# Performance work log

Hardware: AMD Instinct MI355X
Metric: run time of the kernel (lower is better)

## Reference

```python
import jax, jax.numpy as jnp
import numpy as np

C = 256
CQK = C // 8  # query/key channel dim from Conv3d(in, in//8, 1)


def setup_inputs() -> dict:
    key = jax.random.key(0)
    ks = jax.random.split(key, 8)
    B, D, H, W = 2, 16, 16, 16
    x = jax.random.normal(ks[0], (B, C, D, H, W), dtype=jnp.float32)
    s = 1.0 / np.sqrt(C)
    q_w = jax.random.normal(ks[1], (CQK, C), dtype=jnp.float32) * s
    q_b = jax.random.normal(ks[2], (CQK,), dtype=jnp.float32) * 0.01
    k_w = jax.random.normal(ks[3], (CQK, C), dtype=jnp.float32) * s
    k_b = jax.random.normal(ks[4], (CQK,), dtype=jnp.float32) * 0.01
    v_w = jax.random.normal(ks[5], (C, C), dtype=jnp.float32) * s
    v_b = jax.random.normal(ks[6], (C,), dtype=jnp.float32) * 0.01
    gamma = jax.random.normal(ks[7], (1,), dtype=jnp.float32)
    return {"x": x, "q_w": q_w, "q_b": q_b, "k_w": k_w, "k_b": k_b,
            "v_w": v_w, "v_b": v_b, "gamma": gamma}


def reference(x, q_w, q_b, k_w, k_b, v_w, v_b, gamma):
    B, Cc, D, H, W = x.shape
    N = D * H * W
    xf = x.reshape(B, Cc, N)  # [B, C, N]
    # 1x1x1 Conv3d == channel-mixing matmul
    q = jnp.einsum('oc,bcn->bon', q_w, xf) + q_b[None, :, None]  # [B, C/8, N]
    k = jnp.einsum('oc,bcn->bon', k_w, xf) + k_b[None, :, None]  # [B, C/8, N]
    v = jnp.einsum('oc,bcn->bon', v_w, xf) + v_b[None, :, None]  # [B, C, N]
    # attention[b, i, j] = sum_c q[b, c, i] * k[b, c, j]
    attn = jnp.einsum('bci,bcj->bij', q, k)  # [B, N, N]
    attn = jax.nn.softmax(attn, axis=-1)
    # out[b, c, i] = sum_j v[b, c, j] * attn[b, i, j]
    out = jnp.einsum('bcj,bij->bci', v, attn)  # [B, C, N]
    out = out.reshape(B, Cc, D, H, W)
    return gamma[0] * out + x
```

## Files before the change

kernel.cpp:

```cpp
#include <hip/hip_runtime.h>

#define C_DIM 256
#define CQK   32
#define N_DIM 4096
#define B_DIM 2

typedef __attribute__((ext_vector_type(8))) short bf16x8;
typedef __attribute__((ext_vector_type(4))) float f32x4;

__device__ __forceinline__ unsigned short f2bf(float f) {
    union { float f; unsigned u; } v; v.f = f;
    unsigned r = v.u + 0x7FFFu + ((v.u >> 16) & 1u);
    return (unsigned short)(r >> 16);
}
__device__ __forceinline__ unsigned pk2(float a, float b) {
    return (unsigned)f2bf(a) | ((unsigned)f2bf(b) << 16);
}
__device__ __forceinline__ unsigned pk2t(float a, float b) {
    union { float f; unsigned u; } ua, ub; ua.f = a; ub.f = b;
    return __builtin_amdgcn_perm(ub.u, ua.u, 0x07060302u);
}
#define EXP2(x) __builtin_amdgcn_exp2f(x)
#define MFMA(A, B, C) __builtin_amdgcn_mfma_f32_16x16x32_bf16((A), (B), (C), 0, 0, 0)

__global__ __launch_bounds__(256) void wconv(
    const float* __restrict__ q_w, const float* __restrict__ q_b,
    const float* __restrict__ k_w, const float* __restrict__ k_b,
    const float* __restrict__ v_w, const float* __restrict__ v_b,
    unsigned short* __restrict__ wbf, float* __restrict__ biasf)
{
    const float LOG2E = 1.4426950408889634f;
    int o = blockIdx.x, c = threadIdx.x;
    float w;
    if (o < 32)       w = q_w[o * C_DIM + c] * LOG2E;
    else if (o < 64)  w = k_w[(o - 32) * C_DIM + c];
    else              w = v_w[(o - 64) * C_DIM + c];
    wbf[o * C_DIM + c] = f2bf(w);
    if (c == 0) biasf[o] = (o < 32) ? q_b[o] * LOG2E
                         : (o < 64) ? k_b[o - 32] : v_b[o - 64];
}

__global__ __launch_bounds__(256, 2) void qkv_proj(
    const float* __restrict__ x, const unsigned short* __restrict__ wbf,
    const float* __restrict__ biasf,
    unsigned short* __restrict__ qT, unsigned short* __restrict__ kT,
    unsigned short* __restrict__ vbf)
{
    __shared__ __align__(16) unsigned short xsT[16 * 264];
    __shared__ __align__(16) unsigned short qkbuf[2][16 * 36];
    __shared__ __align__(16) unsigned short vbb[256 * 20];
    const int t  = threadIdx.x;
    const int b  = blockIdx.x >> 8;
    const int n0 = (blockIdx.x & 255) * 16;

    {
        int n4 = t & 3, cq = t >> 2;
        const float* xp = x + ((size_t)(b * C_DIM + cq * 4)) * N_DIM + n0 + n4 * 4;
        float4 r0 = *(const float4*)xp;
        float4 r1 = *(const float4*)(xp + N_DIM);
        float4 r2 = *(const float4*)(xp + 2 * N_DIM);
        float4 r3 = *(const float4*)(xp + 3 * N_DIM);
        float a0[4], a1[4], a2[4], a3[4];
        *(float4*)a0 = r0; *(float4*)a1 = r1; *(float4*)a2 = r2; *(float4*)a3 = r3;
        #pragma unroll
        for (int k = 0; k < 4; ++k) {
            uint2 pw;
            pw.x = pk2(a0[k], a1[k]);
            pw.y = pk2(a2[k], a3[k]);
            *(uint2*)&xsT[(n4 * 4 + k) * 264 + cq * 4] = pw;
        }
    }
    __syncthreads();

    const int w = t >> 6, lid = t & 63, lr = lid & 15, lq = lid >> 4;
    f32x4 acc[5] = {};
    #pragma unroll
    for (int ks = 0; ks < 8; ++ks) {
        bf16x8 xb = *(const bf16x8*)&xsT[lr * 264 + ks * 32 + lq * 8];
        #pragma unroll
        for (int u = 0; u < 5; ++u) {
            int gm = w * 5 + u;
            bf16x8 af = *(const bf16x8*)&wbf[(gm * 16 + lr) * C_DIM + ks * 32 + lq * 8];
            acc[u] = MFMA(af, xb, acc[u]);
        }
    }
    #pragma unroll
    for (int u = 0; u < 5; ++u) {
        int gm = w * 5 + u;
        float bv[4];
        *(float4*)bv = *(const float4*)&biasf[gm * 16 + lq * 4];
        if (gm >= 4) {
            int vc = (gm - 4) * 16 + lq * 4;
            #pragma unroll
            for (int r = 0; r < 4; ++r)
                vbb[(vc + r) * 20 + lr] = f2bf(acc[u][r] + bv[r]);
        } else {
            int sel = gm >> 1, half = gm & 1;
            uint2 pw;
            pw.x = pk2(acc[u][0] + bv[0], acc[u][1] + bv[1]);
            pw.y = pk2(acc[u][2] + bv[2], acc[u][3] + bv[3]);
            *(uint2*)&qkbuf[sel][lr * 36 + half * 16 + lq * 4] = pw;
        }
    }
    __syncthreads();
    if (t < 128) {
        int sel = t >> 6, idx = t & 63;
        int n = idx >> 2, ch8 = (idx & 3) * 8;
        const unsigned short* src = &qkbuf[sel][n * 36 + ch8];
        uint2 a = *(const uint2*)src;
        uint2 c = *(const uint2*)(src + 4);
        unsigned short* dst = (sel ? kT : qT) + ((size_t)b * N_DIM + n0 + n) * CQK + ch8;
        uint4 st; st.x = a.x; st.y = a.y; st.z = c.x; st.w = c.y;
        *(uint4*)dst = st;
    }
    {
        const unsigned short* src = &vbb[t * 20];
        uint2 a = *(const uint2*)(src + 0);
        uint2 bq = *(const uint2*)(src + 4);
        uint2 c = *(const uint2*)(src + 8);
        uint2 d = *(const uint2*)(src + 12);
        unsigned short* dst = vbf +
            ((((size_t)(b * 4 + (t >> 6)) * 128 + (n0 >> 5)) * 64 + (t & 63)) * 32
             + (n0 & 31));
        uint4 s0; s0.x = a.x; s0.y = a.y; s0.z = bq.x; s0.w = bq.y;
        uint4 s1; s1.x = c.x; s1.y = c.y; s1.z = d.x; s1.w = d.y;
        *(uint4*)dst = s0;
        *(uint4*)(dst + 8) = s1;
    }
}

__global__ __launch_bounds__(256, 2) void attn_kernel(
    const unsigned short* __restrict__ qT, const unsigned short* __restrict__ kT,
    const unsigned short* __restrict__ vbf, const float* __restrict__ x,
    const float* __restrict__ gamma, float* __restrict__ out)
{
    __shared__ __align__(16) char smem[40960 + 1536];
    unsigned short* pbase = (unsigned short*)smem;
    float* obuf = (float*)smem;
    float* lbuf = (float*)(smem + 40960);

    const int t  = threadIdx.x;
    const int b  = blockIdx.x >> 8;
    const int qt = (blockIdx.x >> 2) & 63;
    const int cs = blockIdx.x & 3;
    const int i0 = qt * 64;
    const int w = t >> 6, lid = t & 63, lr = lid & 15, lq = lid >> 4;

    const unsigned short* qTb = qT + (size_t)b * N_DIM * CQK;
    const unsigned short* kTb = kT + (size_t)b * N_DIM * CQK;
    const unsigned short* vtb = vbf + (size_t)(b * 4 + cs) * 128 * 2048;

    unsigned short* pW0 = pbase + (w * 2 + 0) * (64 * 40);
    unsigned short* pW1 = pbase + (w * 2 + 1) * (64 * 40);

    bf16x8 bq[4];
    #pragma unroll
    for (int it = 0; it < 4; ++it)
        bq[it] = *(const bf16x8*)&qTb[(i0 + it * 16 + lr) * CQK + lq * 8];

    f32x4 oa[4][4] = {};
    float lp[4] = {};

    const int jwbase = w * 1024;
    const int vlane = lr * 32 + lq * 8;

    bf16x8 akc0 = *(const bf16x8*)&kTb[(jwbase + lr) * CQK + lq * 8];
    bf16x8 akc1 = *(const bf16x8*)&kTb[(jwbase + 16 + lr) * CQK + lq * 8];
    bf16x8 avU[4];

    {
        const unsigned short* vt0 = vtb + (size_t)(w * 32) * 2048;
        #pragma unroll
        for (int ct = 0; ct < 4; ++ct)
            avU[ct] = *(const bf16x8*)&vt0[ct * 512 + vlane];
        bf16x8 akn0 = *(const bf16x8*)&kTb[(jwbase + 32 + lr) * CQK + lq * 8];
        bf16x8 akn1 = *(const bf16x8*)&kTb[(jwbase + 32 + 16 + lr) * CQK + lq * 8];
        const f32x4 z = {};
        #pragma unroll
        for (int it = 0; it < 4; ++it) {
            f32x4 s0 = MFMA(akc0, bq[it], z);
            f32x4 s1 = MFMA(akc1, bq[it], z);
            float e0 = EXP2(s0[0]), e1 = EXP2(s0[1]), e2 = EXP2(s0[2]), e3 = EXP2(s0[3]);
            float f0 = EXP2(s1[0]), f1 = EXP2(s1[1]), f2 = EXP2(s1[2]), f3 = EXP2(s1[3]);
            lp[it] += ((e0 + e1) + (e2 + e3)) + ((f0 + f1) + (f2 + f3));
            uint2 pw0; pw0.x = pk2t(e0, e1); pw0.y = pk2t(e2, e3);
            uint2 pw1; pw1.x = pk2t(f0, f1); pw1.y = pk2t(f2, f3);
            unsigned short* prow = pW0 + (it * 16 + lr) * 40;
            *(uint2*)&prow[lq * 4]      = pw0;
            *(uint2*)&prow[16 + lq * 4] = pw1;
        }
        akc0 = akn0; akc1 = akn1;
    }

    #pragma unroll 2
    for (int k = 1; k < 32; ++k) {
        const int jn = jwbase + ((k + 1) & 31) * 32;
        const unsigned short* vtk = vtb + (size_t)(w * 32 + k) * 2048;
        bf16x8 avI[4];
        #pragma unroll
        for (int ct = 0; ct < 4; ++ct)
            avI[ct] = *(const bf16x8*)&vtk[ct * 512 + vlane];
        bf16x8 akn0 = *(const bf16x8*)&kTb[(jn + lr) * CQK + lq * 8];
        bf16x8 akn1 = *(const bf16x8*)&kTb[(jn + 16 + lr) * CQK + lq * 8];
        const unsigned short* pR = (k & 1) ? pW0 : pW1;
        bf16x8 bp[4];
        #pragma unroll
        for (int it = 0; it < 4; ++it)
            bp[it] = *(const bf16x8*)&pR[(it * 16 + lr) * 40 + lq * 8];
        const f32x4 z = {};
        f32x4 s[4][2];
        #pragma unroll
        for (int it = 0; it < 4; ++it) {
            s[it][0] = MFMA(akc0, bq[it], z);
            s[it][1] = MFMA(akc1, bq[it], z);
        }
        #pragma unroll
        for (int it = 0; it < 4; ++it)
            #pragma unroll
            for (int ct = 0; ct < 4; ++ct)
                oa[ct][it] = MFMA(avU[ct], bp[it], oa[ct][it]);
        unsigned short* pWc = (k & 1) ? pW1 : pW0;
        #pragma unroll
        for (int it = 0; it < 4; ++it) {
            float e0 = EXP2(s[it][0][0]), e1 = EXP2(s[it][0][1]);
            float e2 = EXP2(s[it][0][2]), e3 = EXP2(s[it][0][3]);
            float f0 = EXP2(s[it][1][0]), f1 = EXP2(s[it][1][1]);
            float f2 = EXP2(s[it][1][2]), f3 = EXP2(s[it][1][3]);
            lp[it] += ((e0 + e1) + (e2 + e3)) + ((f0 + f1) + (f2 + f3));
            uint2 pw0; pw0.x = pk2t(e0, e1); pw0.y = pk2t(e2, e3);
            uint2 pw1; pw1.x = pk2t(f0, f1); pw1.y = pk2t(f2, f3);
            unsigned short* prow = pWc + (it * 16 + lr) * 40;
            *(uint2*)&prow[lq * 4]      = pw0;
            *(uint2*)&prow[16 + lq * 4] = pw1;
        }
        akc0 = akn0; akc1 = akn1;
        #pragma unroll
        for (int ct = 0; ct < 4; ++ct) avU[ct] = avI[ct];
    }

    {
        bf16x8 bp[4];
        #pragma unroll
        for (int it = 0; it < 4; ++it)
            bp[it] = *(const bf16x8*)&pW1[(it * 16 + lr) * 40 + lq * 8];
        #pragma unroll
        for (int it = 0; it < 4; ++it)
            #pragma unroll
            for (int ct = 0; ct < 4; ++ct)
                oa[ct][it] = MFMA(avU[ct], bp[it], oa[ct][it]);
    }

    #pragma unroll
    for (int it = 0; it < 4; ++it) {
        lp[it] += __shfl_xor(lp[it], 16);
        lp[it] += __shfl_xor(lp[it], 32);
    }
    if (lq == 0) {
        #pragma unroll
        for (int it = 0; it < 4; ++it)
            lbuf[w * 64 + it * 16 + lr] = lp[it];
    }
    __syncthreads();

    for (int ph = 0; ph < 4; ++ph) {
        if (w == ph) {
            #pragma unroll
            for (int ct = 0; ct < 4; ++ct)
                #pragma unroll
                for (int it = 0; it < 4; ++it)
                    #pragma unroll
                    for (int r = 0; r < 4; ++r) {
                        int addr = (ct * 16 + lq * 4 + r) * 68 + it * 16 + lr;
                        if (ph == 0) obuf[addr]  = oa[ct][it][r];
                        else         obuf[addr] += oa[ct][it][r];
                    }
        }
        __syncthreads();
    }
    if (t < 64) {
        float l = lbuf[t] + lbuf[64 + t] + lbuf[128 + t] + lbuf[192 + t];
        lbuf[256 + t] = 1.f / l;
    }
    __syncthreads();

    const float g = gamma[0];
    const int c0 = cs * 64;
    const int cc = t >> 2;
    const int ic = (t & 3) * 16;
    const size_t rowbase = ((size_t)b * C_DIM + c0 + cc) * N_DIM + i0 + ic;
    #pragma unroll
    for (int k = 0; k < 4; ++k) {
        float4 ov4 = *(const float4*)&obuf[cc * 68 + ic + k * 4];
        float4 li  = *(const float4*)&lbuf[256 + ic + k * 4];
        float4 xv  = *(const float4*)(x + rowbase + k * 4);
        float4 ov;
        ov.x = g * ov4.x * li.x + xv.x;
        ov.y = g * ov4.y * li.y + xv.y;
        ov.z = g * ov4.z * li.z + xv.z;
        ov.w = g * ov4.w * li.w + xv.w;
        *(float4*)(out + rowbase + k * 4) = ov;
    }
}

extern "C" void kernel_launch(void* const* d_in, const int* in_sizes, int n_in,
                              void* d_out, int out_size, void* d_ws, size_t ws_size,
                              hipStream_t stream) {
    const float* x     = (const float*)d_in[0];
    const float* q_w   = (const float*)d_in[1];
    const float* q_b   = (const float*)d_in[2];
    const float* k_w   = (const float*)d_in[3];
    const float* k_b   = (const float*)d_in[4];
    const float* v_w   = (const float*)d_in[5];
    const float* v_b   = (const float*)d_in[6];
    const float* gamma = (const float*)d_in[7];
    float* out = (float*)d_out;

    char* ws = (char*)d_ws;
    unsigned short* qT    = (unsigned short*)(ws);
    unsigned short* kT    = (unsigned short*)(ws + 524288);
    unsigned short* vbf   = (unsigned short*)(ws + 1048576);
    unsigned short* wbf   = (unsigned short*)(ws + 5242880);
    float*          biasf = (float*)(ws + 5406720);

    hipLaunchKernelGGL(wconv, dim3(320), dim3(256), 0, stream,
                       q_w, q_b, k_w, k_b, v_w, v_b, wbf, biasf);
    hipLaunchKernelGGL(qkv_proj, dim3(B_DIM * 256), dim3(256), 0, stream,
                       x, wbf, biasf, qT, kT, vbf);
    hipLaunchKernelGGL(attn_kernel, dim3(B_DIM * 64 * 4), dim3(256), 0, stream,
                       qT, kT, vbf, x, gamma, out);
}
```

Measured before the change: 122.5 us.

## Double query tile and wave count per attention block, drop software pipelining

The attention kernel now processes 128 queries per block with 8 waves (512 threads), each wave covering 512 keys instead of 1024. This halves the number of blocks and the redundant K/V loads per query. The double-buffered P tile and the software-pipelined loop, where the QK MFMA for step k overlapped the PV MFMA for step k-1, are replaced by a simple sequential loop with a single P buffer per wave. Costs are more accumulator registers (8 row tiles), lower occupancy from 512-thread blocks with a larger LDS footprint, less instruction-level overlap, and more serialized phases in the cross-wave output reduction.

```diff
diff --git a/kernel.cpp b/kernel.cpp
--- a/kernel.cpp
+++ b/kernel.cpp
@@ -129,55 +129,55 @@
     }
 }
 
-__global__ __launch_bounds__(256, 2) void attn_kernel(
+__global__ __launch_bounds__(512, 2) void attn_kernel(
     const unsigned short* __restrict__ qT, const unsigned short* __restrict__ kT,
     const unsigned short* __restrict__ vbf, const float* __restrict__ x,
     const float* __restrict__ gamma, float* __restrict__ out)
 {
-    __shared__ __align__(16) char smem[40960 + 1536];
+    __shared__ __align__(16) char smem[81920 + 4608];
     unsigned short* pbase = (unsigned short*)smem;
     float* obuf = (float*)smem;
-    float* lbuf = (float*)(smem + 40960);
+    float* lbuf = (float*)(smem + 81920);
 
     const int t  = threadIdx.x;
-    const int b  = blockIdx.x >> 8;
-    const int qt = (blockIdx.x >> 2) & 63;
+    const int b  = blockIdx.x >> 7;
+    const int qt = (blockIdx.x >> 2) & 31;
     const int cs = blockIdx.x & 3;
-    const int i0 = qt * 64;
+    const int i0 = qt * 128;
     const int w = t >> 6, lid = t & 63, lr = lid & 15, lq = lid >> 4;
 
     const unsigned short* qTb = qT + (size_t)b * N_DIM * CQK;
     const unsigned short* kTb = kT + (size_t)b * N_DIM * CQK;
     const unsigned short* vtb = vbf + (size_t)(b * 4 + cs) * 128 * 2048;
 
-    unsigned short* pW0 = pbase + (w * 2 + 0) * (64 * 40);
-    unsigned short* pW1 = pbase + (w * 2 + 1) * (64 * 40);
-
-    bf16x8 bq[4];
-    #pragma unroll
-    for (int it = 0; it < 4; ++it)
+    unsigned short* pW = pbase + w * (128 * 40);
+
+    bf16x8 bq[8];
+    #pragma unroll
+    for (int it = 0; it < 8; ++it)
         bq[it] = *(const bf16x8*)&qTb[(i0 + it * 16 + lr) * CQK + lq * 8];
 
-    f32x4 oa[4][4] = {};
-    float lp[4] = {};
-
-    const int jwbase = w * 1024;
+    f32x4 oa[4][8] = {};
+    float lp[8] = {};
+
+    const int jwbase = w * 512;
     const int vlane = lr * 32 + lq * 8;
 
     bf16x8 akc0 = *(const bf16x8*)&kTb[(jwbase + lr) * CQK + lq * 8];
     bf16x8 akc1 = *(const bf16x8*)&kTb[(jwbase + 16 + lr) * CQK + lq * 8];
-    bf16x8 avU[4];
-
-    {
-        const unsigned short* vt0 = vtb + (size_t)(w * 32) * 2048;
+
+    for (int k = 0; k < 16; ++k) {
+        const unsigned short* vtk = vtb + (size_t)(w * 16 + k) * 2048;
+        bf16x8 avU[4];
         #pragma unroll
         for (int ct = 0; ct < 4; ++ct)
-            avU[ct] = *(const bf16x8*)&vt0[ct * 512 + vlane];
-        bf16x8 akn0 = *(const bf16x8*)&kTb[(jwbase + 32 + lr) * CQK + lq * 8];
-        bf16x8 akn1 = *(const bf16x8*)&kTb[(jwbase + 32 + 16 + lr) * CQK + lq * 8];
+            avU[ct] = *(const bf16x8*)&vtk[ct * 512 + vlane];
+        const int jn = jwbase + ((k + 1) & 15) * 32;
+        bf16x8 akn0 = *(const bf16x8*)&kTb[(jn + lr) * CQK + lq * 8];
+        bf16x8 akn1 = *(const bf16x8*)&kTb[(jn + 16 + lr) * CQK + lq * 8];
         const f32x4 z = {};
         #pragma unroll
-        for (int it = 0; it < 4; ++it) {
+        for (int it = 0; it < 8; ++it) {
             f32x4 s0 = MFMA(akc0, bq[it], z);
             f32x4 s1 = MFMA(akc1, bq[it], z);
             float e0 = EXP2(s0[0]), e1 = EXP2(s0[1]), e2 = EXP2(s0[2]), e3 = EXP2(s0[3]);
@@ -185,113 +185,64 @@
             lp[it] += ((e0 + e1) + (e2 + e3)) + ((f0 + f1) + (f2 + f3));
             uint2 pw0; pw0.x = pk2t(e0, e1); pw0.y = pk2t(e2, e3);
             uint2 pw1; pw1.x = pk2t(f0, f1); pw1.y = pk2t(f2, f3);
-            unsigned short* prow = pW0 + (it * 16 + lr) * 40;
+            unsigned short* prow = pW + (it * 16 + lr) * 40;
             *(uint2*)&prow[lq * 4]      = pw0;
             *(uint2*)&prow[16 + lq * 4] = pw1;
         }
-        akc0 = akn0; akc1 = akn1;
-    }
-
-    #pragma unroll 2
-    for (int k = 1; k < 32; ++k) {
-        const int jn = jwbase + ((k + 1) & 31) * 32;
-        const unsigned short* vtk = vtb + (size_t)(w * 32 + k) * 2048;
-        bf16x8 avI[4];
-        #pragma unroll
-        for (int ct = 0; ct < 4; ++ct)
-            avI[ct] = *(const bf16x8*)&vtk[ct * 512 + vlane];
-        bf16x8 akn0 = *(const bf16x8*)&kTb[(jn + lr) * CQK + lq * 8];
-        bf16x8 akn1 = *(const bf16x8*)&kTb[(jn + 16 + lr) * CQK + lq * 8];
-        const unsigned short* pR = (k & 1) ? pW0 : pW1;
-        bf16x8 bp[4];
-        #pragma unroll
-        for (int it = 0; it < 4; ++it)
-            bp[it] = *(const bf16x8*)&pR[(it * 16 + lr) * 40 + lq * 8];
-        const f32x4 z = {};
-        f32x4 s[4][2];
-        #pragma unroll
-        for (int it = 0; it < 4; ++it) {
-            s[it][0] = MFMA(akc0, bq[it], z);
-            s[it][1] = MFMA(akc1, bq[it], z);
-        }
-        #pragma unroll
-        for (int it = 0; it < 4; ++it)
+        #pragma unroll
+        for (int it = 0; it < 8; ++it) {
+            bf16x8 bp = *(const bf16x8*)&pW[(it * 16 + lr) * 40 + lq * 8];
             #pragma unroll
             for (int ct = 0; ct < 4; ++ct)
-                oa[ct][it] = MFMA(avU[ct], bp[it], oa[ct][it]);
-        unsigned short* pWc = (k & 1) ? pW1 : pW0;
-        #pragma unroll
-        for (int it = 0; it < 4; ++it) {
-            float e0 = EXP2(s[it][0][0]), e1 = EXP2(s[it][0][1]);
-            float e2 = EXP2(s[it][0][2]), e3 = EXP2(s[it][0][3]);
-            float f0 = EXP2(s[it][1][0]), f1 = EXP2(s[it][1][1]);
-            float f2 = EXP2(s[it][1][2]), f3 = EXP2(s[it][1][3]);
-            lp[it] += ((e0 + e1) + (e2 + e3)) + ((f0 + f1) + (f2 + f3));
-            uint2 pw0; pw0.x = pk2t(e0, e1); pw0.y = pk2t(e2, e3);
-            uint2 pw1; pw1.x = pk2t(f0, f1); pw1.y = pk2t(f2, f3);
-            unsigned short* prow = pWc + (it * 16 + lr) * 40;
-            *(uint2*)&prow[lq * 4]      = pw0;
-            *(uint2*)&prow[16 + lq * 4] = pw1;
+                oa[ct][it] = MFMA(avU[ct], bp, oa[ct][it]);
         }
         akc0 = akn0; akc1 = akn1;
-        #pragma unroll
-        for (int ct = 0; ct < 4; ++ct) avU[ct] = avI[ct];
-    }
-
-    {
-        bf16x8 bp[4];
-        #pragma unroll
-        for (int it = 0; it < 4; ++it)
-            bp[it] = *(const bf16x8*)&pW1[(it * 16 + lr) * 40 + lq * 8];
-        #pragma unroll
-        for (int it = 0; it < 4; ++it)
-            #pragma unroll
-            for (int ct = 0; ct < 4; ++ct)
-                oa[ct][it] = MFMA(avU[ct], bp[it], oa[ct][it]);
-    }
-
-    #pragma unroll
-    for (int it = 0; it < 4; ++it) {
+    }
+
+    #pragma unroll
+    for (int it = 0; it < 8; ++it) {
         lp[it] += __shfl_xor(lp[it], 16);
         lp[it] += __shfl_xor(lp[it], 32);
     }
     if (lq == 0) {
         #pragma unroll
-        for (int it = 0; it < 4; ++it)
-            lbuf[w * 64 + it * 16 + lr] = lp[it];
-    }
-    __syncthreads();
-
-    for (int ph = 0; ph < 4; ++ph) {
+        for (int it = 0; it < 8; ++it)
+            lbuf[w * 128 + it * 16 + lr] = lp[it];
+    }
+    __syncthreads();
+
+    for (int ph = 0; ph < 8; ++ph) {
         if (w == ph) {
             #pragma unroll
             for (int ct = 0; ct < 4; ++ct)
                 #pragma unroll
-                for (int it = 0; it < 4; ++it)
+                for (int it = 0; it < 8; ++it)
                     #pragma unroll
                     for (int r = 0; r < 4; ++r) {
-                        int addr = (ct * 16 + lq * 4 + r) * 68 + it * 16 + lr;
+                        int addr = (ct * 16 + lq * 4 + r) * 132 + it * 16 + lr;
                         if (ph == 0) obuf[addr]  = oa[ct][it][r];
                         else         obuf[addr] += oa[ct][it][r];
                     }
         }
         __syncthreads();
     }
-    if (t < 64) {
-        float l = lbuf[t] + lbuf[64 + t] + lbuf[128 + t] + lbuf[192 + t];
-        lbuf[256 + t] = 1.f / l;
+    if (t < 128) {
+        float l = lbuf[t];
+        #pragma unroll
+        for (int ww = 1; ww < 8; ++ww) l += lbuf[ww * 128 + t];
+        lbuf[1024 + t] = 1.f / l;
     }
     __syncthreads();
 
     const float g = gamma[0];
     const int c0 = cs * 64;
-    const int cc = t >> 2;
-    const int ic = (t & 3) * 16;
+    const int cc = t >> 3;
+    const int ic = (t & 7) * 16;
     const size_t rowbase = ((size_t)b * C_DIM + c0 + cc) * N_DIM + i0 + ic;
     #pragma unroll
     for (int k = 0; k < 4; ++k) {
-        float4 ov4 = *(const float4*)&obuf[cc * 68 + ic + k * 4];
-        float4 li  = *(const float4*)&lbuf[256 + ic + k * 4];
+        float4 ov4 = *(const float4*)&obuf[cc * 132 + ic + k * 4];
+        float4 li  = *(const float4*)&lbuf[1024 + ic + k * 4];
         float4 xv  = *(const float4*)(x + rowbase + k * 4);
         float4 ov;
         ov.x = g * ov4.x * li.x + xv.x;
@@ -326,6 +277,6 @@
                        q_w, q_b, k_w, k_b, v_w, v_b, wbf, biasf);
     hipLaunchKernelGGL(qkv_proj, dim3(B_DIM * 256), dim3(256), 0, stream,
                        x, wbf, biasf, qT, kT, vbf);
-    hipLaunchKernelGGL(attn_kernel, dim3(B_DIM * 64 * 4), dim3(256), 0, stream,
+    hipLaunchKernelGGL(attn_kernel, dim3(B_DIM * 32 * 4), dim3(512), 0, stream,
                        qT, kT, vbf, x, gamma, out);
 }
```

After: 178.0 us. +45.3%, slower.
